# Kernel tuning notes

Hardware: AMD Instinct MI355X
Metric: run time of the kernel (lower is better)

The kernel has to match this reference:

```python
import jax, jax.numpy as jnp
import numpy as np

L = 4        # num_layers
D = 64       # in_channels == hidden_channels
OUT = 1      # out_channels
N = 50000    # nodes
E = 800000   # edges
G = 64       # graphs in batch
EPS = 1e-5


def setup_inputs() -> dict:
    key = jax.random.key(0)
    ks = jax.random.split(key, 16)
    s = 1.0 / np.sqrt(D)
    inp = {
        "x": jax.random.normal(ks[0], (N, D), jnp.float32),
        "edge_index": jax.random.randint(ks[1], (2, E), 0, N, jnp.int32),
        "batch": jnp.sort(jax.random.randint(ks[2], (N,), 0, G, jnp.int32)),
        # per-layer GNLayer params (stacked over L)
        "Wm1": jax.random.uniform(ks[3], (L, D, D), jnp.float32, -s, s),
        "bm1": jnp.zeros((L, D), jnp.float32),
        "Wm2": jax.random.uniform(ks[4], (L, D, D), jnp.float32, -s, s),
        "bm2": jnp.zeros((L, D), jnp.float32),
        "Wr": jax.random.uniform(ks[5], (L, D, D), jnp.float32, -s, s),
        "br": jnp.zeros((L, D), jnp.float32),
        "a_conv": jnp.full((L,), 0.25, jnp.float32),     # PReLU slopes
        "gamma": jnp.ones((L, D), jnp.float32),
        "beta": jnp.zeros((L, D), jnp.float32),
        # MLP head
        "Wh1": jax.random.uniform(ks[6], (D, D), jnp.float32, -s, s),
        "bh1": jnp.zeros((D,), jnp.float32),
        "Wh2": jax.random.uniform(ks[7], (D, OUT), jnp.float32, -s, s),
        "bh2": jnp.zeros((OUT,), jnp.float32),
        "a_head": jnp.float32(0.25),
    }
    return inp


def _prelu(v, a):
    return jnp.where(v >= 0, v, a * v)


def reference(x, edge_index, batch, Wm1, bm1, Wm2, bm2, Wr, br, a_conv,
              gamma, beta, Wh1, bh1, Wh2, bh2, a_head):
    src, dst = edge_index[0], edge_index[1]
    h = x
    for i in range(L):
        # GNLayer: message MLP on source features, sum-aggregate at dst, + root transform
        m = jax.nn.relu(h[src] @ Wm1[i] + bm1[i]) @ Wm2[i] + bm2[i]   # [E, D]
        agg = jax.ops.segment_sum(m, dst, num_segments=N)              # [N, D]
        h = agg + h @ Wr[i] + br[i]
        # PReLU
        h = _prelu(h, a_conv[i])
        # BatchNorm over the node dimension (training-mode batch stats)
        mu = jnp.mean(h, axis=0)
        var = jnp.var(h, axis=0)
        h = gamma[i] * (h - mu) * jax.lax.rsqrt(var + EPS) + beta[i]
    # global_mean_pool over graphs
    sums = jax.ops.segment_sum(h, batch, num_segments=G)               # [G, D]
    cnts = jax.ops.segment_sum(jnp.ones((N, 1), h.dtype), batch, num_segments=G)
    g = sums / jnp.maximum(cnts, 1.0)
    # MLP head
    out = _prelu(g @ Wh1 + bh1, a_head) @ Wh2 + bh2                    # [G, OUT]
    return out
```

## Files before the change

kernel.cpp:

```cpp
#include <hip/hip_runtime.h>
#include <hip/hip_fp16.h>

#define D 64


__global__ __launch_bounds__(256) void hist_kernel(const int* __restrict__ dst,
                                                   int* __restrict__ cnt, int E) {
  int e = blockIdx.x * 256 + threadIdx.x;
  if (e < E) atomicAdd(&cnt[dst[e]], 1);
}

__global__ __launch_bounds__(1024) void scan_partial_kernel(const int* __restrict__ cnt,
                                                            int* __restrict__ bsum, int N) {
  __shared__ int lds[1024];
  int i = blockIdx.x * 1024 + threadIdx.x;
  lds[threadIdx.x] = (i < N) ? cnt[i] : 0;
  __syncthreads();
  for (int off = 512; off > 0; off >>= 1) {
    if (threadIdx.x < off) lds[threadIdx.x] += lds[threadIdx.x + off];
    __syncthreads();
  }
  if (threadIdx.x == 0) bsum[blockIdx.x] = lds[0];
}

__global__ void scan_bsum_kernel(int* __restrict__ bsum, int nb,
                                 int* __restrict__ row_ptr, int N, int E) {
  int tid = threadIdx.x;
  int o = (tid < nb) ? bsum[tid] : 0;
  int v = o;
  for (int off = 1; off < 64; off <<= 1) {
    int t = __shfl_up(v, off, 64);
    if (tid >= off) v += t;
  }
  if (tid < nb) bsum[tid] = v - o;
  if (tid == 0) row_ptr[N] = E;
}

__global__ __launch_bounds__(1024) void scan_final_kernel(const int* __restrict__ cnt,
                                                          const int* __restrict__ bsum,
                                                          int* __restrict__ row_ptr,
                                                          int* __restrict__ cursor, int N) {
  __shared__ int lds[1024];
  int tid = threadIdx.x;
  int i = blockIdx.x * 1024 + tid;
  int v = (i < N) ? cnt[i] : 0;
  lds[tid] = v;
  __syncthreads();
  for (int off = 1; off < 1024; off <<= 1) {
    int t = (tid >= off) ? lds[tid - off] : 0;
    __syncthreads();
    lds[tid] += t;
    __syncthreads();
  }
  if (i < N) {
    int excl = bsum[blockIdx.x] + lds[tid] - v;
    row_ptr[i] = excl;
    cursor[i] = excl;
  }
}

__global__ __launch_bounds__(256) void scatter_kernel(const int* __restrict__ srcs,
                                                      const int* __restrict__ dst,
                                                      int* __restrict__ cursor,
                                                      int* __restrict__ csr_src, int E) {
  int e = blockIdx.x * 256 + threadIdx.x;
  if (e < E) {
    int p = atomicAdd(&cursor[dst[e]], 1);
    csr_src[p] = srcs[e];
  }
}


__global__ __launch_bounds__(256, 4) void node_mlp_kernel(
    const float* __restrict__ hin, const float* __restrict__ bnS, const float* __restrict__ bnSS,
    const float* __restrict__ gammaL, const float* __restrict__ betaL,
    const float* __restrict__ W1, const float* __restrict__ b1,
    const float* __restrict__ W2, const float* __restrict__ b2,
    __half* __restrict__ Rout, float* __restrict__ HRout, int N) {
  __shared__ float2 w12[D * D];
  __shared__ float hrow[32][D];
  const int tid = threadIdx.x;
  for (int i = tid; i < D * D; i += 256) w12[i] = make_float2(W1[i], W2[i]);
  const int c = tid & 63;
  const int w = tid >> 6;
  float sc = 1.f, sh = 0.f;
  if (bnS) {
    float invN = 1.f / (float)N;
    float mu = bnS[c] * invN;
    float var = bnSS[c] * invN - mu * mu;
    float s = gammaL[c] * rsqrtf(var + 1e-5f);
    sc = s;
    sh = betaL[c] - mu * s;
  }
  const float bb1 = b1[c], bb2 = b2[c];
  const int ntiles = (N + 31) >> 5;
  for (int t = blockIdx.x; t < ntiles; t += gridDim.x) {
    const int base = t * 32;
    __syncthreads();
#pragma unroll
    for (int j = 0; j < 8; ++j) {
      int r = 4 * j + w;
      int row = base + r;
      float v = (row < N) ? hin[(size_t)row * D + c] : 0.f;
      hrow[r][c] = v * sc + sh;
    }
    __syncthreads();
    float a1[8], a2[8];
#pragma unroll
    for (int j = 0; j < 8; ++j) { a1[j] = bb1; a2[j] = bb2; }
    for (int k = 0; k < D; k += 4) {
      const float2 wa = w12[(k + 0) * D + c];
      const float2 wb = w12[(k + 1) * D + c];
      const float2 wc = w12[(k + 2) * D + c];
      const float2 wd = w12[(k + 3) * D + c];
#pragma unroll
      for (int j = 0; j < 8; ++j) {
        const float4 h4 = *(const float4*)&hrow[w * 8 + j][k];
        a1[j] += h4.x * wa.x + h4.y * wb.x + h4.z * wc.x + h4.w * wd.x;
        a2[j] += h4.x * wa.y + h4.y * wb.y + h4.z * wc.y + h4.w * wd.y;
      }
    }
#pragma unroll
    for (int j = 0; j < 8; ++j) {
      int row = base + w * 8 + j;
      if (row < N) {
        Rout[(size_t)row * D + c] = __float2half(fmaxf(a1[j], 0.f));
        HRout[(size_t)row * D + c] = a2[j];
      }
    }
  }
}


__device__ __forceinline__ float lane_bcast(float v, int lane) {
  return __int_as_float(__builtin_amdgcn_readlane(__float_as_int(v), lane));
}
__device__ __forceinline__ int lane_bcast_i(int v, int lane) {
  return __builtin_amdgcn_readlane(v, lane);
}

__global__ __launch_bounds__(256) void agg_kernel(const int* __restrict__ row_ptr,
                                                  const int* __restrict__ csr_src,
                                                  const __half* __restrict__ Rm,
                                                  const float* __restrict__ HRm,
                                                  const float* __restrict__ W2m,
                                                  const float* __restrict__ b2m,
                                                  const float* __restrict__ aconv,
                                                  float* __restrict__ hout,
                                                  float* __restrict__ bnsum,
                                                  float* __restrict__ bnsumsq, int N) {
  __shared__ float w2[D * D];
  __shared__ float red[4][D];
  __shared__ float red2[4][D];
  const int tid = threadIdx.x;
  const int c = tid & 63;
  const int w = tid >> 6;
  const int q = c & 15;
  const int eg = c >> 4;
  for (int i = tid; i < D * D; i += 256) w2[i] = W2m[i];
  const float alpha = *aconv;
  const float bb = b2m[c];
  const int NW = gridDim.x * 4;
  float psum = 0.f, psumsq = 0.f;
  __syncthreads();

  int n = blockIdx.x * 4 + w;
  int e0 = 0, e1 = 0, idx = 0;
  if (n < N) {
    e0 = row_ptr[n];
    e1 = row_ptr[n + 1];
    int m = e1 - e0;
    if (m > 64) m = 64;
    if (m > 0) idx = csr_src[e0 + (c < m ? c : m - 1)];
  }
  while (n < N) {
    const int n2 = n + NW;
    int e0n = 0, e1n = 0, idxn = 0;
    if (n2 < N) {
      e0n = row_ptr[n2];
      e1n = row_ptr[n2 + 1];
      int mn = e1n - e0n;
      if (mn > 64) mn = 64;
      if (mn > 0) idxn = csr_src[e0n + (c < mn ? c : mn - 1)];
    }
    const int deg = e1 - e0;
    float acc0 = 0.f, acc1 = 0.f, acc2 = 0.f, acc3 = 0.f;
    int kb = 0;
    int curidx = idx;
    while (kb < deg) {
      int m = deg - kb;
      if (m > 64) m = 64;
      if (kb > 0) curidx = csr_src[e0 + kb + (c < m ? c : m - 1)];
      int j = 0;
      for (; j + 3 < m; j += 4) {
        const int s = __shfl(curidx, j + eg, 64);
        const uint2 rv = *(const uint2*)(Rm + (size_t)s * D + (q << 2));
        const float2 f01 = __half22float2(*(const __half2*)&rv.x);
        const float2 f23 = __half22float2(*(const __half2*)&rv.y);
        acc0 += f01.x;
        acc1 += f01.y;
        acc2 += f23.x;
        acc3 += f23.y;
      }
      for (; j < m; ++j) {
        const int s = lane_bcast_i(curidx, j);
        if (eg == 0) {
          const uint2 rv = *(const uint2*)(Rm + (size_t)s * D + (q << 2));
          const float2 f01 = __half22float2(*(const __half2*)&rv.x);
          const float2 f23 = __half22float2(*(const __half2*)&rv.y);
          acc0 += f01.x;
          acc1 += f01.y;
          acc2 += f23.x;
          acc3 += f23.y;
        }
      }
      kb += m;
    }
    acc0 += __shfl_xor(acc0, 16, 64);
    acc1 += __shfl_xor(acc1, 16, 64);
    acc2 += __shfl_xor(acc2, 16, 64);
    acc3 += __shfl_xor(acc3, 16, 64);
    acc0 += __shfl_xor(acc0, 32, 64);
    acc1 += __shfl_xor(acc1, 32, 64);
    acc2 += __shfl_xor(acc2, 32, 64);
    acc3 += __shfl_xor(acc3, 32, 64);
    const float degf = (float)deg;
    float o0 = bb * degf + HRm[(size_t)n * D + c];
    float o1 = 0.f, o2 = 0.f, o3 = 0.f;
#pragma unroll
    for (int kk = 0; kk < D; kk += 4) {
      const int src = kk >> 2;
      o0 += lane_bcast(acc0, src) * w2[(kk + 0) * D + c];
      o1 += lane_bcast(acc1, src) * w2[(kk + 1) * D + c];
      o2 += lane_bcast(acc2, src) * w2[(kk + 2) * D + c];
      o3 += lane_bcast(acc3, src) * w2[(kk + 3) * D + c];
    }
    const float o = (o0 + o1) + (o2 + o3);
    const float h2 = (o >= 0.f) ? o : alpha * o;
    hout[(size_t)n * D + c] = h2;
    psum += h2;
    psumsq += h2 * h2;
    n = n2;
    e0 = e0n;
    e1 = e1n;
    idx = idxn;
  }
  red[w][c] = psum;
  red2[w][c] = psumsq;
  __syncthreads();
  if (w == 0) {
    float s = red[0][c] + red[1][c] + red[2][c] + red[3][c];
    float ss = red2[0][c] + red2[1][c] + red2[2][c] + red2[3][c];
    atomicAdd(&bnsum[c], s);
    atomicAdd(&bnsumsq[c], ss);
  }
}


__global__ __launch_bounds__(256) void pool_head_kernel(
    const float* __restrict__ h, const float* __restrict__ bnS, const float* __restrict__ bnSS,
    const float* __restrict__ gammaL, const float* __restrict__ betaL,
    const int* __restrict__ batch, const float* __restrict__ Wh1, const float* __restrict__ bh1,
    const float* __restrict__ Wh2, const float* __restrict__ bh2,
    const float* __restrict__ ahead, float* __restrict__ out, int N) {
  const int g = blockIdx.x;
  const int tid = threadIdx.x;
  const int c = tid & 63;
  const int w = tid >> 6;
  float sc, sh;
  {
    float invN = 1.f / (float)N;
    float mu = bnS[c] * invN;
    float var = bnSS[c] * invN - mu * mu;
    float s = gammaL[c] * rsqrtf(var + 1e-5f);
    sc = s;
    sh = betaL[c] - mu * s;
  }
  int s0, s1;
  {
    int lo = 0, hi = N;
    while (lo < hi) { int mid = (lo + hi) >> 1; if (batch[mid] < g) lo = mid + 1; else hi = mid; }
    s0 = lo;
    lo = s0; hi = N;
    while (lo < hi) { int mid = (lo + hi) >> 1; if (batch[mid] < g + 1) lo = mid + 1; else hi = mid; }
    s1 = lo;
  }
  float sum = 0.f;
  for (int r = s0 + w; r < s1; r += 4) sum += h[(size_t)r * D + c] * sc + sh;
  __shared__ float red[4][D];
  __shared__ float mean[D];
  red[w][c] = sum;
  __syncthreads();
  if (tid < D) {
    float cnt = (float)(s1 - s0);
    mean[c] = (red[0][c] + red[1][c] + red[2][c] + red[3][c]) / fmaxf(cnt, 1.0f);
  }
  __syncthreads();
  if (tid < D) {
    int j = tid;
    float a = bh1[j];
#pragma unroll
    for (int k = 0; k < D; ++k) a += mean[k] * Wh1[k * D + j];
    float al = *ahead;
    float v = (a >= 0.f) ? a : al * a;
    float pval = v * Wh2[j];
    for (int off = 32; off > 0; off >>= 1) pval += __shfl_down(pval, off, 64);
    if (j == 0) out[g] = pval + bh2[0];
  }
}


extern "C" void kernel_launch(void* const* d_in, const int* in_sizes, int n_in,
                              void* d_out, int out_size, void* d_ws, size_t ws_size,
                              hipStream_t stream) {
  const float* x = (const float*)d_in[0];
  const int* ei = (const int*)d_in[1];
  const int* batch = (const int*)d_in[2];
  const float* Wm1 = (const float*)d_in[3];
  const float* bm1 = (const float*)d_in[4];
  const float* Wm2 = (const float*)d_in[5];
  const float* bm2 = (const float*)d_in[6];
  const float* Wr = (const float*)d_in[7];
  const float* br = (const float*)d_in[8];
  const float* aconv = (const float*)d_in[9];
  const float* gamma = (const float*)d_in[10];
  const float* beta = (const float*)d_in[11];
  const float* Wh1 = (const float*)d_in[12];
  const float* bh1 = (const float*)d_in[13];
  const float* Wh2 = (const float*)d_in[14];
  const float* bh2 = (const float*)d_in[15];
  const float* ahead = (const float*)d_in[16];

  const int N = in_sizes[0] / D;
  const int E = in_sizes[1] / 2;
  const int L = in_sizes[3] / (D * D);
  const int G = out_size;

  const int* srcs = ei;
  const int* dsts = ei + E;

  char* p = (char*)d_ws;
  auto alloc = [&](size_t bytes) {
    char* r = p;
    p += (bytes + 255) & ~(size_t)255;
    return r;
  };
  int* row_ptr = (int*)alloc((size_t)(N + 1) * 4);
  int* cursor = (int*)alloc((size_t)N * 4);
  float* bnsum = (float*)alloc((size_t)L * D * 4 * 2);
  float* bnsumsq = bnsum + (size_t)L * D;
  const size_t zero_bytes = (size_t)((char*)(bnsum + 2 * L * D) - (char*)row_ptr);
  int* bsum = (int*)alloc(64 * 4);
  int* csr_src = (int*)alloc((size_t)E * 4);
  __half* Rbuf = (__half*)alloc((size_t)N * D * 2);
  float* HRbuf = (float*)alloc((size_t)N * D * 4);
  float* hbuf = (float*)alloc((size_t)N * D * 4);

  hipMemsetAsync(row_ptr, 0, zero_bytes, stream);

  const int nb = (N + 1023) / 1024;
  hist_kernel<<<(E + 255) / 256, 256, 0, stream>>>(dsts, cursor, E);
  scan_partial_kernel<<<nb, 1024, 0, stream>>>(cursor, bsum, N);
  scan_bsum_kernel<<<1, 64, 0, stream>>>(bsum, nb, row_ptr, N, E);
  scan_final_kernel<<<nb, 1024, 0, stream>>>(cursor, bsum, row_ptr, cursor, N);
  scatter_kernel<<<(E + 255) / 256, 256, 0, stream>>>(srcs, dsts, cursor, csr_src, E);

  const int ntiles = (N + 31) / 32;
  const int mlp_blocks = (ntiles < 768) ? ntiles : 768;

  const float* hin = x;
  const float* bnS = nullptr;
  const float* bnSS = nullptr;
  const float* gmL = nullptr;
  const float* btL = nullptr;
  for (int l = 0; l < L; ++l) {
    node_mlp_kernel<<<mlp_blocks, 256, 0, stream>>>(hin, bnS, bnSS, gmL, btL,
                                                    Wm1 + (size_t)l * D * D, bm1 + l * D,
                                                    Wr + (size_t)l * D * D, br + l * D,
                                                    Rbuf, HRbuf, N);
    agg_kernel<<<2048, 256, 0, stream>>>(row_ptr, csr_src, Rbuf, HRbuf,
                                         Wm2 + (size_t)l * D * D, bm2 + l * D, aconv + l,
                                         hbuf, bnsum + l * D, bnsumsq + l * D, N);
    hin = hbuf;
    bnS = bnsum + l * D;
    bnSS = bnsumsq + l * D;
    gmL = gamma + l * D;
    btL = beta + l * D;
  }

  pool_head_kernel<<<G, 256, 0, stream>>>(hbuf, bnS, bnSS, gmL, btL, batch,
                                          Wh1, bh1, Wh2, bh2, ahead, (float*)d_out, N);
}
```

Baseline: 596.3 us.

## Process two destination nodes per wavefront in aggregation kernel

Measured after the change: 574.0 us. 3.7% less time.

```diff
diff --git a/kernel.cpp b/kernel.cpp
--- a/kernel.cpp
+++ b/kernel.cpp
@@ -135,9 +135,6 @@
 __device__ __forceinline__ float lane_bcast(float v, int lane) {
   return __int_as_float(__builtin_amdgcn_readlane(__float_as_int(v), lane));
 }
-__device__ __forceinline__ int lane_bcast_i(int v, int lane) {
-  return __builtin_amdgcn_readlane(v, lane);
-}
 
 __global__ __launch_bounds__(256) void agg_kernel(const int* __restrict__ row_ptr,
                                                   const int* __restrict__ csr_src,
@@ -156,56 +153,42 @@
   const int c = tid & 63;
   const int w = tid >> 6;
   const int q = c & 15;
-  const int eg = c >> 4;
+  const int slot = c >> 4;
+  const int half = slot >> 1;
+  const int eslot = slot & 1;
+  const int l32 = c & 31;
   for (int i = tid; i < D * D; i += 256) w2[i] = W2m[i];
   const float alpha = *aconv;
   const float bb = b2m[c];
-  const int NW = gridDim.x * 4;
+  const int NWAVES = gridDim.x * 4;
   float psum = 0.f, psumsq = 0.f;
   __syncthreads();
 
-  int n = blockIdx.x * 4 + w;
-  int e0 = 0, e1 = 0, idx = 0;
-  if (n < N) {
-    e0 = row_ptr[n];
-    e1 = row_ptr[n + 1];
-    int m = e1 - e0;
-    if (m > 64) m = 64;
-    if (m > 0) idx = csr_src[e0 + (c < m ? c : m - 1)];
-  }
-  while (n < N) {
-    const int n2 = n + NW;
-    int e0n = 0, e1n = 0, idxn = 0;
-    if (n2 < N) {
-      e0n = row_ptr[n2];
-      e1n = row_ptr[n2 + 1];
-      int mn = e1n - e0n;
-      if (mn > 64) mn = 64;
-      if (mn > 0) idxn = csr_src[e0n + (c < mn ? c : mn - 1)];
-    }
-    const int deg = e1 - e0;
+  const int npairs = (N + 1) >> 1;
+  for (int p = blockIdx.x * 4 + w; p < npairs; p += NWAVES) {
+    const int nA = 2 * p;
+    const int nB = nA + 1;
+    const int myn = nA + half;
+    int e0 = 0, deg = 0;
+    if (myn < N) {
+      e0 = row_ptr[myn];
+      deg = row_ptr[myn + 1] - e0;
+    }
+    const int degA = __shfl(deg, 0, 64);
+    const int degB = __shfl(deg, 32, 64);
+    const int dm = degA > degB ? degA : degB;
     float acc0 = 0.f, acc1 = 0.f, acc2 = 0.f, acc3 = 0.f;
-    int kb = 0;
-    int curidx = idx;
-    while (kb < deg) {
-      int m = deg - kb;
-      if (m > 64) m = 64;
-      if (kb > 0) curidx = csr_src[e0 + kb + (c < m ? c : m - 1)];
-      int j = 0;
-      for (; j + 3 < m; j += 4) {
-        const int s = __shfl(curidx, j + eg, 64);
-        const uint2 rv = *(const uint2*)(Rm + (size_t)s * D + (q << 2));
-        const float2 f01 = __half22float2(*(const __half2*)&rv.x);
-        const float2 f23 = __half22float2(*(const __half2*)&rv.y);
-        acc0 += f01.x;
-        acc1 += f01.y;
-        acc2 += f23.x;
-        acc3 += f23.y;
-      }
-      for (; j < m; ++j) {
-        const int s = lane_bcast_i(curidx, j);
-        if (eg == 0) {
-          const uint2 rv = *(const uint2*)(Rm + (size_t)s * D + (q << 2));
+    for (int base = 0; base < dm; base += 32) {
+      const int rem = deg - base;
+      const int m_my = rem < 32 ? rem : 32;
+      int idxreg = 0;
+      if (m_my > 0) idxreg = csr_src[e0 + base + (l32 < m_my ? l32 : m_my - 1)];
+      const int itop = (dm - base) < 32 ? (dm - base) : 32;
+      for (int kk = 0; kk < itop; kk += 2) {
+        const int k = kk + eslot;
+        const int sidx = __shfl(idxreg, half * 32 + k, 64);
+        if (k < m_my) {
+          const uint2 rv = *(const uint2*)(Rm + (size_t)sidx * D + (q << 2));
           const float2 f01 = __half22float2(*(const __half2*)&rv.x);
           const float2 f23 = __half22float2(*(const __half2*)&rv.y);
           acc0 += f01.x;
@@ -214,36 +197,43 @@
           acc3 += f23.y;
         }
       }
-      kb += m;
     }
     acc0 += __shfl_xor(acc0, 16, 64);
     acc1 += __shfl_xor(acc1, 16, 64);
     acc2 += __shfl_xor(acc2, 16, 64);
     acc3 += __shfl_xor(acc3, 16, 64);
-    acc0 += __shfl_xor(acc0, 32, 64);
-    acc1 += __shfl_xor(acc1, 32, 64);
-    acc2 += __shfl_xor(acc2, 32, 64);
-    acc3 += __shfl_xor(acc3, 32, 64);
-    const float degf = (float)deg;
-    float o0 = bb * degf + HRm[(size_t)n * D + c];
-    float o1 = 0.f, o2 = 0.f, o3 = 0.f;
+    float oA0 = 0.f, oA1 = 0.f, oA2 = 0.f, oA3 = 0.f;
+    float oB0 = 0.f, oB1 = 0.f, oB2 = 0.f, oB3 = 0.f;
 #pragma unroll
     for (int kk = 0; kk < D; kk += 4) {
       const int src = kk >> 2;
-      o0 += lane_bcast(acc0, src) * w2[(kk + 0) * D + c];
-      o1 += lane_bcast(acc1, src) * w2[(kk + 1) * D + c];
-      o2 += lane_bcast(acc2, src) * w2[(kk + 2) * D + c];
-      o3 += lane_bcast(acc3, src) * w2[(kk + 3) * D + c];
-    }
-    const float o = (o0 + o1) + (o2 + o3);
-    const float h2 = (o >= 0.f) ? o : alpha * o;
-    hout[(size_t)n * D + c] = h2;
-    psum += h2;
-    psumsq += h2 * h2;
-    n = n2;
-    e0 = e0n;
-    e1 = e1n;
-    idx = idxn;
+      const float wv0 = w2[(kk + 0) * D + c];
+      const float wv1 = w2[(kk + 1) * D + c];
+      const float wv2 = w2[(kk + 2) * D + c];
+      const float wv3 = w2[(kk + 3) * D + c];
+      oA0 += lane_bcast(acc0, src) * wv0;
+      oA1 += lane_bcast(acc1, src) * wv1;
+      oA2 += lane_bcast(acc2, src) * wv2;
+      oA3 += lane_bcast(acc3, src) * wv3;
+      oB0 += lane_bcast(acc0, 32 + src) * wv0;
+      oB1 += lane_bcast(acc1, 32 + src) * wv1;
+      oB2 += lane_bcast(acc2, 32 + src) * wv2;
+      oB3 += lane_bcast(acc3, 32 + src) * wv3;
+    }
+    {
+      const float o = ((oA0 + oA1) + (oA2 + oA3)) + bb * (float)degA + HRm[(size_t)nA * D + c];
+      const float h2 = (o >= 0.f) ? o : alpha * o;
+      hout[(size_t)nA * D + c] = h2;
+      psum += h2;
+      psumsq += h2 * h2;
+    }
+    if (nB < N) {
+      const float o = ((oB0 + oB1) + (oB2 + oB3)) + bb * (float)degB + HRm[(size_t)nB * D + c];
+      const float h2 = (o >= 0.f) ? o : alpha * o;
+      hout[(size_t)nB * D + c] = h2;
+      psum += h2;
+      psumsq += h2 * h2;
+    }
   }
   red[w][c] = psum;
   red2[w][c] = psumsq;
@@ -366,7 +356,6 @@
   scatter_kernel<<<(E + 255) / 256, 256, 0, stream>>>(srcs, dsts, cursor, csr_src, E);
 
   const int ntiles = (N + 31) / 32;
-  const int mlp_blocks = (ntiles < 768) ? ntiles : 768;
 
   const float* hin = x;
   const float* bnS = nullptr;
@@ -374,10 +363,10 @@
   const float* gmL = nullptr;
   const float* btL = nullptr;
   for (int l = 0; l < L; ++l) {
-    node_mlp_kernel<<<mlp_blocks, 256, 0, stream>>>(hin, bnS, bnSS, gmL, btL,
-                                                    Wm1 + (size_t)l * D * D, bm1 + l * D,
-                                                    Wr + (size_t)l * D * D, br + l * D,
-                                                    Rbuf, HRbuf, N);
+    node_mlp_kernel<<<ntiles, 256, 0, stream>>>(hin, bnS, bnSS, gmL, btL,
+                                                Wm1 + (size_t)l * D * D, bm1 + l * D,
+                                                Wr + (size_t)l * D * D, br + l * D,
+                                                Rbuf, HRbuf, N);
     agg_kernel<<<2048, 256, 0, stream>>>(row_ptr, csr_src, Rbuf, HRbuf,
                                          Wm2 + (size_t)l * D * D, bm2 + l * D, aconv + l,
                                          hbuf, bnsum + l * D, bnsumsq + l * D, N);
```
